# Kernel optimization log

Hardware: AMD Instinct MI355X
Metric: run time of the kernel (lower is better)

The kernel has to match this reference:

```python
import jax, jax.numpy as jnp
import numpy as np

N_HEADS = 32
KV_HEADS = 8
HEAD_DIM = 64
THETA = 10000.0


def _rope_tables(L, head_dim, dtype):
    freqs = 1.0 / (THETA ** (jnp.arange(0, head_dim, 2, dtype=jnp.float32) / head_dim))
    phases = jnp.outer(jnp.arange(L, dtype=jnp.float32), freqs)  # [L, head_dim//2]
    phases = jnp.concatenate([phases, phases], axis=-1)          # [L, head_dim]
    return jnp.cos(phases).astype(dtype), jnp.sin(phases).astype(dtype)


def _rotate_half(x):
    x1, x2 = jnp.split(x, 2, axis=-1)
    return jnp.concatenate([-x2, x1], axis=-1)


def setup_inputs() -> dict:
    key = jax.random.key(0)
    ks = jax.random.split(key, 5)
    B, L, D = 2, 2048, 2048
    kv_dim = KV_HEADS * HEAD_DIM
    s = 0.02
    return {
        "x": jax.random.normal(ks[0], (B, L, D), jnp.float32),
        "wq": jax.random.normal(ks[1], (D, D), jnp.float32) * s,
        "wk": jax.random.normal(ks[2], (kv_dim, D), jnp.float32) * s,
        "wv": jax.random.normal(ks[3], (kv_dim, D), jnp.float32) * s,
        "wo": jax.random.normal(ks[4], (D, D), jnp.float32) * s,
    }


def reference(x, wq, wk, wv, wo):
    B, L, D = x.shape
    rep = N_HEADS // KV_HEADS
    cos, sin = _rope_tables(L, HEAD_DIM, x.dtype)  # [L, hd]

    # projections (torch Linear: y = x @ W.T)
    q = jnp.einsum('bld,ed->ble', x, wq).reshape(B, L, N_HEADS, HEAD_DIM).transpose(0, 2, 1, 3)   # [B,H,L,hd]
    k = jnp.einsum('bld,ed->ble', x, wk).reshape(B, L, KV_HEADS, HEAD_DIM).transpose(0, 2, 1, 3)  # [B,Hk,L,hd]
    v = jnp.einsum('bld,ed->ble', x, wv).reshape(B, L, KV_HEADS, HEAD_DIM).transpose(0, 2, 1, 3)

    # RoPE (broadcast over batch/heads)
    q = cos * q + _rotate_half(q) * sin
    k = cos * k + _rotate_half(k) * sin

    # GQA attention without materializing repeated K/V: group query heads per kv head
    qg = q.reshape(B, KV_HEADS, rep, L, HEAD_DIM)
    scale = 1.0 / jnp.sqrt(jnp.asarray(HEAD_DIM, x.dtype))
    scores = jnp.einsum('bkrqd,bkld->bkrql', qg, k) * scale  # [B,Hk,rep,L,L]
    causal = jnp.tril(jnp.ones((L, L), bool))
    scores = jnp.where(causal, scores, jnp.asarray(-jnp.inf, scores.dtype))
    attn = jax.nn.softmax(scores, axis=-1)
    out = jnp.einsum('bkrql,bkld->bkrqd', attn, v)           # [B,Hk,rep,L,hd]
    out = out.reshape(B, N_HEADS, L, HEAD_DIM).transpose(0, 2, 1, 3).reshape(B, L, D)
    return jnp.einsum('ble,de->bld', out, wo)
```

## Files before the change

kernel.cpp:

```cpp
#include <hip/hip_runtime.h>

typedef __attribute__((ext_vector_type(8))) __bf16 bf16x8;
typedef __attribute__((ext_vector_type(8))) ushort u16x8;
typedef __attribute__((ext_vector_type(4))) float f32x4;
typedef __attribute__((ext_vector_type(16))) float f32x16;

#define MFMA16(a, b, c) __builtin_amdgcn_mfma_f32_16x16x32_bf16(a, b, c, 0, 0, 0)
#define MFMA32(a, b, c) __builtin_amdgcn_mfma_f32_32x32x16_bf16(a, b, c, 0, 0, 0)

__device__ __forceinline__ ushort f2bf(float f) {
    union { float f; unsigned u; } v; v.f = f;
    unsigned r = v.u + 0x7FFFu + ((v.u >> 16) & 1u);
    return (ushort)(r >> 16);
}
__device__ __forceinline__ float bf2f(ushort b) {
    union { unsigned u; float f; } v; v.u = ((unsigned)b) << 16; return v.f;
}
__device__ __forceinline__ int cvtpk(float lo, float hi) {
    int r; asm("v_cvt_pk_bf16_f32 %0, %1, %2" : "=v"(r) : "v"(lo), "v"(hi)); return r;
}
__device__ __forceinline__ float fexp2(float x) {
    float r; asm("v_exp_f32 %0, %1" : "=v"(r) : "v"(x)); return r;
}
__device__ __forceinline__ void gload_lds16(const void* g, void* l) {
    __builtin_amdgcn_global_load_lds((const __attribute__((address_space(1))) void*)g,
                                     (__attribute__((address_space(3))) void*)l, 16, 0, 0);
}

__device__ __forceinline__ int swz8(int row, int g) {
    return row * 64 + (((g) ^ (row & 7)) << 3);
}
__device__ __forceinline__ int swz16(int row, int g) {
    return row * 128 + (((g) ^ (row & 15)) << 3);
}

__device__ __forceinline__ void stage64(const ushort* __restrict__ g, int rs,
                                        char* lds, int tid) {
    const int r = tid >> 3;
    const int c8 = ((tid & 7) ^ (r & 7)) << 3;
    const int wid = tid >> 6;
    gload_lds16(g + (size_t)r * rs + c8, lds + wid * 1024);
    gload_lds16(g + (size_t)(r + 32) * rs + c8, lds + 4096 + wid * 1024);
}

__device__ __forceinline__ void stageV128(const ushort* __restrict__ g, char* lds, int tid) {
    const int w = tid >> 6, l = tid & 63;
    const int g16 = l & 15;
#pragma unroll
    for (int j = 0; j < 4; ++j) {
        const int r = w * 16 + j * 4 + (l >> 4);
        gload_lds16(g + (size_t)r * 2048 + ((g16 ^ (r & 15)) << 3), lds + w * 4096 + j * 1024);
    }
}

__global__ void cvt_all(const float* __restrict__ x,  const float* __restrict__ wq,
                        const float* __restrict__ wk, const float* __restrict__ wv,
                        const float* __restrict__ wo, ushort* __restrict__ xb,
                        ushort* __restrict__ wcat, ushort* __restrict__ wob,
                        float* __restrict__ cosT, float* __restrict__ sinT) {
    int i = blockIdx.x * 256 + threadIdx.x;
    if (i >= 4718592) {
        int id = i - 4718592;
        if (id < 65536) {
            int fi = id >> 11, l = id & 2047;
            float freq = __expf(-(float)fi * (9.210340371976184f / 32.0f));
            float ph = (float)l * freq;
            cosT[id] = cosf(ph);
            sinT[id] = sinf(ph);
        }
        return;
    }
    const float* src; ushort* dst; int off;
    if (i < 2097152)      { src = x;  dst = xb;             off = i; }
    else if (i < 3145728) { src = wq; dst = wcat;           off = i - 2097152; }
    else if (i < 3407872) { src = wk; dst = wcat + 4194304; off = i - 3145728; }
    else if (i < 3670016) { src = wv; dst = wcat + 5242880; off = i - 3407872; }
    else                  { src = wo; dst = wob;            off = i - 3670016; }
    float4 v = ((const float4*)src)[off];
    ushort4 o;
    o.x = f2bf(v.x); o.y = f2bf(v.y); o.z = f2bf(v.z); o.w = f2bf(v.w);
    ((ushort4*)dst)[off] = o;
}

__global__ __launch_bounds__(512, 2) void gemmQKV(const ushort* __restrict__ A,
                                                  const ushort* __restrict__ B,
                                                  ushort* __restrict__ qkv,
                                                  ushort* __restrict__ vt,
                                                  const float* __restrict__ cosT,
                                                  const float* __restrict__ sinT,
                                                  int M, int N, int K, int gx) {
    constexpr int MF = 8, NF = 4;
    constexpr int ABUF = 256 * 32, BBUF = 256 * 32;
    extern __shared__ __align__(16) ushort sm[];
    ushort* sA = sm;
    ushort* sB = sm + 3 * ABUF;
    const int tid = threadIdx.x, lane = tid & 63, wid = tid >> 6;
    const int wr = wid >> 2, wc = wid & 3;
    const int lr = lane & 15, lg = lane >> 4;
    const int nwg = gridDim.x, bid = blockIdx.x;
    const int swz = (bid & 7) * (nwg >> 3) + (bid >> 3);
    const int m0 = (swz / gx) * 256, n0 = (swz % gx) * 256;
    const int NT = K >> 5;
    const int csrc = ((tid & 3) ^ ((tid >> 3) & 3)) << 3;
    const int co = ((lg ^ ((lr >> 1) & 3)) << 3);
    const ushort* gAt = A + (size_t)(m0 + (tid >> 2)) * K + csrc;
    const ushort* gBt = B + (size_t)(n0 + (tid >> 2)) * K + csrc;

    auto stgA = [&](int t, int buf) {
        const ushort* g = gAt + t * 32;
        char* ld = (char*)(sA + buf * ABUF) + wid * 1024;
        gload_lds16(g, ld);
        gload_lds16(g + (size_t)128 * K, ld + 8192);
    };
    auto stgB = [&](int t, int buf) {
        const ushort* g = gBt + t * 32;
        char* ld = (char*)(sB + buf * BBUF) + wid * 1024;
        gload_lds16(g, ld);
        gload_lds16(g + (size_t)128 * K, ld + 8192);
    };

    f32x4 acc[MF][NF] = {};
    stgA(0, 0); stgB(0, 0); stgA(1, 1); stgB(1, 1);
    asm volatile("s_waitcnt vmcnt(4)" ::: "memory");
    __builtin_amdgcn_s_barrier();

    int cur = 0, stg = 2;
    for (int t = 0; t < NT; ++t) {
        const ushort* Ac = sA + cur * ABUF + (wr * 128) * 32 + co;
        const ushort* Bc = sB + cur * BBUF + (wc * 64) * 32 + co;
        bf16x8 bfr[NF], af[MF / 2];
#pragma unroll
        for (int nf = 0; nf < NF; ++nf) bfr[nf] = *(const bf16x8*)&Bc[(nf * 16 + lr) * 32];
#pragma unroll
        for (int mf = 0; mf < MF / 2; ++mf) af[mf] = *(const bf16x8*)&Ac[(mf * 16 + lr) * 32];
        if (t + 2 < NT) stgA(t + 2, stg);
        __builtin_amdgcn_s_barrier();
        __builtin_amdgcn_s_setprio(1);
#pragma unroll
        for (int mf = 0; mf < MF / 2; ++mf)
#pragma unroll
            for (int nf = 0; nf < NF; ++nf)
                acc[mf][nf] = MFMA16(af[mf], bfr[nf], acc[mf][nf]);
        __builtin_amdgcn_s_setprio(0);
        __builtin_amdgcn_s_barrier();
        bf16x8 af2[MF / 2];
#pragma unroll
        for (int mf = 0; mf < MF / 2; ++mf)
            af2[mf] = *(const bf16x8*)&Ac[((mf + MF / 2) * 16 + lr) * 32];
        if (t + 2 < NT) {
            stgB(t + 2, stg);
            asm volatile("s_waitcnt vmcnt(4)" ::: "memory");
        } else {
            asm volatile("s_waitcnt vmcnt(0)" ::: "memory");
        }
        __builtin_amdgcn_s_barrier();
        __builtin_amdgcn_s_setprio(1);
#pragma unroll
        for (int mf = 0; mf < MF / 2; ++mf)
#pragma unroll
            for (int nf = 0; nf < NF; ++nf)
                acc[mf + MF / 2][nf] = MFMA16(af2[mf], bfr[nf], acc[mf + MF / 2][nf]);
        __builtin_amdgcn_s_setprio(0);
        __builtin_amdgcn_s_barrier();
        cur = (cur == 2) ? 0 : cur + 1;
        stg = (stg == 2) ? 0 : stg + 1;
    }

    const int r0 = m0 + wr * 128 + lg * 4;
    const int c0 = n0 + wc * 64 + lr;
    const int wavecol = n0 + wc * 64;
    if (wavecol >= 2560) {
        const int kh = (wavecol - 2560) >> 6;
        const int b = m0 >> 11;
        const int l0 = r0 & 2047;
#pragma unroll
        for (int ni = 0; ni < NF; ++ni) {
            const int d = lr + ni * 16;
            ushort* vrow = vt + (size_t)((b * 8 + kh) * 64 + d) * 2048 + l0;
#pragma unroll
            for (int mi = 0; mi < MF; ++mi) {
                ushort4 o;
                o.x = f2bf(acc[mi][ni][0]); o.y = f2bf(acc[mi][ni][1]);
                o.z = f2bf(acc[mi][ni][2]); o.w = f2bf(acc[mi][ni][3]);
                *(ushort4*)(vrow + mi * 16) = o;
            }
        }
    } else {
        const float scale = (wavecol < 2048) ? 0.18033688f : 1.0f;
        const int l0 = r0 & 2047;
#pragma unroll
        for (int ni = 0; ni < NF / 2; ++ni) {
            const int i = ni * 16 + lr;
            const float* cp = cosT + i * 2048 + l0;
            const float* sp = sinT + i * 2048 + l0;
#pragma unroll
            for (int mi = 0; mi < MF; ++mi) {
                float4 cv = *(const float4*)(cp + mi * 16);
                float4 sv = *(const float4*)(sp + mi * 16);
#pragma unroll
                for (int r = 0; r < 4; ++r) {
                    float lo = acc[mi][ni][r], hi = acc[mi][ni + 2][r];
                    float c = ((const float*)&cv)[r], s = ((const float*)&sv)[r];
                    size_t row = (size_t)(r0 + mi * 16 + r) * 3072;
                    qkv[row + c0 + ni * 16]      = f2bf((c * lo - s * hi) * scale);
                    qkv[row + c0 + ni * 16 + 32] = f2bf((c * hi + s * lo) * scale);
                }
            }
        }
    }
}

__global__ __launch_bounds__(512, 2) void gemm64(const ushort* __restrict__ A,
                                                 const ushort* __restrict__ B,
                                                 float* __restrict__ C,
                                                 int M, int N, int K, int gx) {
    extern __shared__ __align__(16) ushort sm[];
    ushort* sA = sm;
    ushort* sB = sm + 32768;
    const int tid = threadIdx.x, lane = tid & 63, wid = tid >> 6;
    const int wr = wid >> 1, wc = wid & 1;
    const int lr = lane & 15, lg = lane >> 4;
    const int nwg = gridDim.x, bid = blockIdx.x;
    const int swz = (bid & 7) * (nwg >> 3) + (bid >> 3);
    const int m0 = (swz / gx) * 256, n0 = (swz % gx) * 128;
    const int NT = K >> 6;
    const int sr = tid >> 3;
    const int sc8 = ((tid & 7) ^ (sr & 7)) << 3;
    const ushort* gAt = A + (size_t)(m0 + sr) * K + sc8;
    const ushort* gBt = B + (size_t)(n0 + sr) * K + sc8;

    auto stgA = [&](int t, int buf) {
        const ushort* g = gAt + t * 64;
        char* ld = (char*)(sA + buf * 16384) + wid * 1024;
#pragma unroll
        for (int s = 0; s < 4; ++s)
            gload_lds16(g + (size_t)(s * 64) * K, ld + s * 8192);
    };
    auto stgB = [&](int t, int buf) {
        const ushort* g = gBt + t * 64;
        char* ld = (char*)(sB + buf * 8192) + wid * 1024;
        gload_lds16(g, ld);
        gload_lds16(g + (size_t)64 * K, ld + 8192);
    };

    f32x4 acc[4][4] = {};
    stgA(0, 0); stgB(0, 0);
    stgA(1, 1); stgB(1, 1);
    asm volatile("s_waitcnt vmcnt(6)" ::: "memory");
    __builtin_amdgcn_s_barrier();

    for (int t = 0; t < NT; ++t) {
        const int c = t & 1;
        const ushort* Ac = sA + c * 16384 + (wr * 64) * 64;
        const ushort* Bc = sB + c * 8192 + (wc * 64) * 64;
        bf16x8 af[4][2], bfr[4][2];
#pragma unroll
        for (int mf = 0; mf < 4; ++mf)
#pragma unroll
            for (int kk = 0; kk < 2; ++kk)
                af[mf][kk] = *(const bf16x8*)&Ac[swz8(mf * 16 + lr, kk * 4 + lg)];
#pragma unroll
        for (int nf = 0; nf < 4; ++nf)
#pragma unroll
            for (int kk = 0; kk < 2; ++kk)
                bfr[nf][kk] = *(const bf16x8*)&Bc[swz8(nf * 16 + lr, kk * 4 + lg)];
        __builtin_amdgcn_s_setprio(1);
#pragma unroll
        for (int mf = 0; mf < 4; ++mf)
#pragma unroll
            for (int nf = 0; nf < 4; ++nf)
#pragma unroll
                for (int kk = 0; kk < 2; ++kk)
                    acc[mf][nf] = MFMA16(af[mf][kk], bfr[nf][kk], acc[mf][nf]);
        __builtin_amdgcn_s_setprio(0);
        __builtin_amdgcn_s_barrier();
        if (t + 2 < NT) {
            stgA(t + 2, c); stgB(t + 2, c);
            asm volatile("s_waitcnt vmcnt(6)" ::: "memory");
        } else {
            asm volatile("s_waitcnt vmcnt(0)" ::: "memory");
        }
        __builtin_amdgcn_s_barrier();
    }

    const int r0 = m0 + wr * 64 + lg * 4;
    const int c0 = n0 + wc * 64 + lr;
#pragma unroll
    for (int mi = 0; mi < 4; ++mi)
#pragma unroll
        for (int ni = 0; ni < 4; ++ni)
#pragma unroll
            for (int r = 0; r < 4; ++r)
                C[(size_t)(r0 + mi * 16 + r) * N + c0 + ni * 16] = acc[mi][ni][r];
}

__global__ __launch_bounds__(256, 2) void attn_k(const ushort* __restrict__ qkv,
                                                 const ushort* __restrict__ vt,
                                                 ushort* __restrict__ attn) {
    extern __shared__ __align__(16) ushort smem[];
    const int tid = threadIdx.x, lane = tid & 63, wid = tid >> 6;
    const int hl = lane >> 5, lq = lane & 31;
    const int p = blockIdx.x;
    const int head = blockIdx.y, b = blockIdx.z;
    const int kh = head >> 2;

    const ushort* Kg = qkv + (size_t)(b * 2048) * 3072 + 2048 + kh * 64;
    const ushort* Vg = vt + (size_t)((b * 8 + kh) * 64) * 2048;

    for (int ph = 0; ph < 2; ++ph) {
        const int qt = ph ? p : 15 - p;
        const int qb = qt << 7;
        const int qw0 = qb + wid * 32;
        const int q_lane = qw0 + lq;
        const int nt = qt + 1;

        bf16x8 qf[4];
        {
            const ushort* qp = qkv + (size_t)(b * 2048 + qw0 + lq) * 3072 + head * 64 + hl * 8;
#pragma unroll
            for (int j = 0; j < 4; ++j) qf[j] = *(const bf16x8*)(qp + j * 16);
        }
        f32x16 o0 = {}, o1 = {};
        float lsum = 0.f;

        stage64(Kg, 3072, (char*)smem, tid);
        stage64(Kg + (size_t)64 * 3072, 3072, (char*)smem + 8192, tid);
        stageV128(Vg, (char*)(smem + 16384), tid);

        for (int it = 0; it < nt; ++it) {
            const int c = it & 1;
            const int kv0 = it << 7;
            const ushort* Kc = smem + c * 8192;
            const ushort* Vc = smem + 16384 + c * 8192;
            if (it + 1 < nt) {
                const int kv1 = kv0 + 128;
                char* kd = (char*)smem + (c ^ 1) * 16384;
                char* vd = (char*)(smem + 16384) + (c ^ 1) * 16384;
                stage64(Kg + (size_t)kv1 * 3072, 3072, kd, tid);
                stage64(Kg + (size_t)(kv1 + 64) * 3072, 3072, kd + 8192, tid);
                stageV128(Vg + kv1, vd, tid);
                asm volatile("s_waitcnt vmcnt(8)" ::: "memory");
            } else {
                asm volatile("s_waitcnt vmcnt(0)" ::: "memory");
            }
            __builtin_amdgcn_s_barrier();

            f32x16 s0 = {}, s1 = {}, s2 = {}, s3 = {};
            __builtin_amdgcn_s_setprio(1);
#pragma unroll
            for (int j = 0; j < 4; ++j) {
                bf16x8 k0 = *(const bf16x8*)&Kc[swz8(lq, j * 2 + hl)];
                bf16x8 k1 = *(const bf16x8*)&Kc[swz8(32 + lq, j * 2 + hl)];
                bf16x8 k2 = *(const bf16x8*)&Kc[swz8(64 + lq, j * 2 + hl)];
                bf16x8 k3 = *(const bf16x8*)&Kc[swz8(96 + lq, j * 2 + hl)];
                s0 = MFMA32(k0, qf[j], s0);
                s1 = MFMA32(k1, qf[j], s1);
                s2 = MFMA32(k2, qf[j], s2);
                s3 = MFMA32(k3, qf[j], s3);
            }
            __builtin_amdgcn_s_setprio(0);

            if (it == qt) {
#pragma unroll
                for (int i = 0; i < 16; ++i) {
                    int r = (i & 3) + ((i >> 2) << 3) + (hl << 2) + kv0;
                    if (r > q_lane)      s0[i] = -1e30f;
                    if (r + 32 > q_lane) s1[i] = -1e30f;
                    if (r + 64 > q_lane) s2[i] = -1e30f;
                    if (r + 96 > q_lane) s3[i] = -1e30f;
                }
            }
#pragma unroll
            for (int i = 0; i < 16; ++i) s0[i] = fexp2(s0[i]);
#pragma unroll
            for (int i = 0; i < 16; ++i) s1[i] = fexp2(s1[i]);
#pragma unroll
            for (int i = 0; i < 16; ++i) s2[i] = fexp2(s2[i]);
#pragma unroll
            for (int i = 0; i < 16; ++i) s3[i] = fexp2(s3[i]);
            f32x16 ts = (s0 + s1) + (s2 + s3);
            float u0 = ts[0] + ts[1], u1 = ts[2] + ts[3], u2 = ts[4] + ts[5], u3 = ts[6] + ts[7];
            float u4 = ts[8] + ts[9], u5 = ts[10] + ts[11], u6 = ts[12] + ts[13], u7 = ts[14] + ts[15];
            float rs = ((u0 + u1) + (u2 + u3)) + ((u4 + u5) + (u6 + u7));
            {
                auto sw = __builtin_amdgcn_permlane32_swap(__float_as_int(rs), __float_as_int(rs), 0, 0);
                rs = __int_as_float(sw[0]) + __int_as_float(sw[1]);
            }
            lsum += rs;

            bf16x8 pf[8];
#define PFB(cc, q0, q1, q2, q3, q4, q5, q6, q7)                                   \
            {                                                                      \
                int pk01 = cvtpk(q0, q1), pk23 = cvtpk(q2, q3);                    \
                int pk45 = cvtpk(q4, q5), pk67 = cvtpk(q6, q7);                    \
                auto sA = __builtin_amdgcn_permlane32_swap(pk01, pk45, 0, 0);      \
                auto sB = __builtin_amdgcn_permlane32_swap(pk23, pk67, 0, 0);      \
                union { int w[4]; bf16x8 v; } u;                                   \
                u.w[0] = sA[0]; u.w[1] = sB[0]; u.w[2] = sA[1]; u.w[3] = sB[1];    \
                pf[cc] = u.v;                                                      \
            }
            PFB(0, s0[0], s0[1], s0[2], s0[3], s0[4], s0[5], s0[6], s0[7])
            PFB(1, s0[8], s0[9], s0[10], s0[11], s0[12], s0[13], s0[14], s0[15])
            PFB(2, s1[0], s1[1], s1[2], s1[3], s1[4], s1[5], s1[6], s1[7])
            PFB(3, s1[8], s1[9], s1[10], s1[11], s1[12], s1[13], s1[14], s1[15])
            PFB(4, s2[0], s2[1], s2[2], s2[3], s2[4], s2[5], s2[6], s2[7])
            PFB(5, s2[8], s2[9], s2[10], s2[11], s2[12], s2[13], s2[14], s2[15])
            PFB(6, s3[0], s3[1], s3[2], s3[3], s3[4], s3[5], s3[6], s3[7])
            PFB(7, s3[8], s3[9], s3[10], s3[11], s3[12], s3[13], s3[14], s3[15])
#undef PFB
            __builtin_amdgcn_s_setprio(1);
#pragma unroll
            for (int cc = 0; cc < 8; ++cc) {
                bf16x8 v0 = *(const bf16x8*)&Vc[swz16(lq, cc * 2 + hl)];
                bf16x8 v1 = *(const bf16x8*)&Vc[swz16(32 + lq, cc * 2 + hl)];
                o0 = MFMA32(v0, pf[cc], o0);
                o1 = MFMA32(v1, pf[cc], o1);
            }
            __builtin_amdgcn_s_setprio(0);
            __builtin_amdgcn_s_barrier();
        }

        __syncthreads();
        ushort* sc = (ushort*)((char*)smem + wid * 4096);
        float inv = 1.0f / lsum;
#pragma unroll
        for (int i = 0; i < 16; i += 2) {
            int d0 = (i & 3) + ((i >> 2) << 3) + (hl << 2);
            int g0 = d0 >> 3, g1 = (d0 + 32) >> 3;
            *(int*)&sc[lq * 64 + ((g0 ^ (lq & 7)) << 3) + (d0 & 7)] = cvtpk(o0[i] * inv, o0[i + 1] * inv);
            *(int*)&sc[lq * 64 + ((g1 ^ (lq & 7)) << 3) + (d0 & 7)] = cvtpk(o1[i] * inv, o1[i + 1] * inv);
        }
        __syncthreads();
        {
            const int q = lane >> 1, db = (lane & 1) << 5;
            const size_t orow = (size_t)(b * 2048 + qb + wid * 32 + q);
#pragma unroll
            for (int j = 0; j < 4; ++j) {
                int g = (db >> 3) + j;
                u16x8 v = *(const u16x8*)&sc[q * 64 + ((g ^ (q & 7)) << 3)];
                *(u16x8*)(attn + orow * 2048 + head * 64 + g * 8) = v;
            }
        }
        __syncthreads();
    }
}

extern "C" void kernel_launch(void* const* d_in, const int* in_sizes, int n_in,
                              void* d_out, int out_size, void* d_ws, size_t ws_size,
                              hipStream_t stream) {
    const float* x  = (const float*)d_in[0];
    const float* wq = (const float*)d_in[1];
    const float* wk = (const float*)d_in[2];
    const float* wv = (const float*)d_in[3];
    const float* wo = (const float*)d_in[4];
    float* out = (float*)d_out;
    char* ws = (char*)d_ws;

    ushort* xb   = (ushort*)(ws);
    ushort* wcat = (ushort*)(ws + 16777216);
    ushort* wob  = (ushort*)(ws + 29360128);
    ushort* qkv  = (ushort*)(ws + 37748736);
    ushort* vt   = (ushort*)(ws + 62914560);
    ushort* attn = (ushort*)(ws + 67108864);
    float*  cosT = (float*)(ws + 83886080);
    float*  sinT = (float*)(ws + 84148224);

    (void)hipFuncSetAttribute((const void*)gemmQKV,
                              hipFuncAttributeMaxDynamicSharedMemorySize, 98304);
    (void)hipFuncSetAttribute((const void*)gemm64,
                              hipFuncAttributeMaxDynamicSharedMemorySize, 98304);
    (void)hipFuncSetAttribute((const void*)attn_k,
                              hipFuncAttributeMaxDynamicSharedMemorySize, 65536);

    cvt_all<<<18688, 256, 0, stream>>>(x, wq, wk, wv, wo, xb, wcat, wob, cosT, sinT);
    gemmQKV<<<192, 512, 98304, stream>>>(xb, wcat, qkv, vt, cosT, sinT, 4096, 3072, 2048, 12);
    attn_k<<<dim3(8, 32, 2), 256, 65536, stream>>>(qkv, vt, attn);
    gemm64<<<256, 512, 98304, stream>>>(attn, wob, out, 4096, 2048, 2048, 16);
}
```

Before: 172.4 us.

## Restructure QKV GEMM to K-step 64 with double-buffered LDS pipeline

The fused QKV projection GEMM now consumes 64-wide K tiles instead of 32, using two LDS buffers instead of three and an XOR swizzle over 8 chunks. Each iteration issues twice as many MFMAs between barriers and prefetches both A and B two stages ahead after the compute, halving the number of loop iterations and barriers. LDS use grows to 128 KB per block, so only one block fits per CU despite the launch bound of 2, which trades occupancy for fewer synchronisations.

```diff
diff --git a/kernel.cpp b/kernel.cpp
--- a/kernel.cpp
+++ b/kernel.cpp
@@ -82,88 +82,97 @@
     ((ushort4*)dst)[off] = o;
 }
 
-__global__ __launch_bounds__(512, 2) void gemmQKV(const ushort* __restrict__ A,
-                                                  const ushort* __restrict__ B,
-                                                  ushort* __restrict__ qkv,
-                                                  ushort* __restrict__ vt,
-                                                  const float* __restrict__ cosT,
-                                                  const float* __restrict__ sinT,
-                                                  int M, int N, int K, int gx) {
-    constexpr int MF = 8, NF = 4;
-    constexpr int ABUF = 256 * 32, BBUF = 256 * 32;
+__global__ __launch_bounds__(512, 2) void gemmQKV64(const ushort* __restrict__ A,
+                                                    const ushort* __restrict__ B,
+                                                    ushort* __restrict__ qkv,
+                                                    ushort* __restrict__ vt,
+                                                    const float* __restrict__ cosT,
+                                                    const float* __restrict__ sinT,
+                                                    int K, int gx) {
     extern __shared__ __align__(16) ushort sm[];
     ushort* sA = sm;
-    ushort* sB = sm + 3 * ABUF;
+    ushort* sB = sm + 32768;
     const int tid = threadIdx.x, lane = tid & 63, wid = tid >> 6;
     const int wr = wid >> 2, wc = wid & 3;
     const int lr = lane & 15, lg = lane >> 4;
     const int nwg = gridDim.x, bid = blockIdx.x;
     const int swz = (bid & 7) * (nwg >> 3) + (bid >> 3);
     const int m0 = (swz / gx) * 256, n0 = (swz % gx) * 256;
-    const int NT = K >> 5;
-    const int csrc = ((tid & 3) ^ ((tid >> 3) & 3)) << 3;
-    const int co = ((lg ^ ((lr >> 1) & 3)) << 3);
-    const ushort* gAt = A + (size_t)(m0 + (tid >> 2)) * K + csrc;
-    const ushort* gBt = B + (size_t)(n0 + (tid >> 2)) * K + csrc;
+    const int NT = K >> 6;
+    const int sr = tid >> 3;
+    const int sc8 = ((tid & 7) ^ (sr & 7)) << 3;
+    const ushort* gAt = A + (size_t)(m0 + sr) * K + sc8;
+    const ushort* gBt = B + (size_t)(n0 + sr) * K + sc8;
 
     auto stgA = [&](int t, int buf) {
-        const ushort* g = gAt + t * 32;
-        char* ld = (char*)(sA + buf * ABUF) + wid * 1024;
-        gload_lds16(g, ld);
-        gload_lds16(g + (size_t)128 * K, ld + 8192);
+        const ushort* g = gAt + t * 64;
+        char* ld = (char*)(sA + buf * 16384) + wid * 1024;
+#pragma unroll
+        for (int s = 0; s < 4; ++s)
+            gload_lds16(g + (size_t)(s * 64) * K, ld + s * 8192);
     };
     auto stgB = [&](int t, int buf) {
-        const ushort* g = gBt + t * 32;
-        char* ld = (char*)(sB + buf * BBUF) + wid * 1024;
-        gload_lds16(g, ld);
-        gload_lds16(g + (size_t)128 * K, ld + 8192);
+        const ushort* g = gBt + t * 64;
+        char* ld = (char*)(sB + buf * 16384) + wid * 1024;
+#pragma unroll
+        for (int s = 0; s < 4; ++s)
+            gload_lds16(g + (size_t)(s * 64) * K, ld + s * 8192);
     };
 
-    f32x4 acc[MF][NF] = {};
-    stgA(0, 0); stgB(0, 0); stgA(1, 1); stgB(1, 1);
-    asm volatile("s_waitcnt vmcnt(4)" ::: "memory");
+    f32x4 acc[8][4] = {};
+    stgA(0, 0); stgB(0, 0);
+    stgA(1, 1); stgB(1, 1);
+    asm volatile("s_waitcnt vmcnt(8)" ::: "memory");
     __builtin_amdgcn_s_barrier();
 
-    int cur = 0, stg = 2;
     for (int t = 0; t < NT; ++t) {
-        const ushort* Ac = sA + cur * ABUF + (wr * 128) * 32 + co;
-        const ushort* Bc = sB + cur * BBUF + (wc * 64) * 32 + co;
-        bf16x8 bfr[NF], af[MF / 2];
-#pragma unroll
-        for (int nf = 0; nf < NF; ++nf) bfr[nf] = *(const bf16x8*)&Bc[(nf * 16 + lr) * 32];
-#pragma unroll
-        for (int mf = 0; mf < MF / 2; ++mf) af[mf] = *(const bf16x8*)&Ac[(mf * 16 + lr) * 32];
-        if (t + 2 < NT) stgA(t + 2, stg);
-        __builtin_amdgcn_s_barrier();
+        const int c = t & 1;
+        const ushort* Ac = sA + c * 16384 + (wr * 128) * 64;
+        const ushort* Bc = sB + c * 16384 + (wc * 64) * 64;
+        bf16x8 bfr[4][2];
+#pragma unroll
+        for (int nf = 0; nf < 4; ++nf)
+#pragma unroll
+            for (int kk = 0; kk < 2; ++kk)
+                bfr[nf][kk] = *(const bf16x8*)&Bc[swz8(nf * 16 + lr, kk * 4 + lg)];
+        bf16x8 af[4][2];
+#pragma unroll
+        for (int mf = 0; mf < 4; ++mf)
+#pragma unroll
+            for (int kk = 0; kk < 2; ++kk)
+                af[mf][kk] = *(const bf16x8*)&Ac[swz8(mf * 16 + lr, kk * 4 + lg)];
         __builtin_amdgcn_s_setprio(1);
 #pragma unroll
-        for (int mf = 0; mf < MF / 2; ++mf)
-#pragma unroll
-            for (int nf = 0; nf < NF; ++nf)
-                acc[mf][nf] = MFMA16(af[mf], bfr[nf], acc[mf][nf]);
+        for (int mf = 0; mf < 4; ++mf)
+#pragma unroll
+            for (int nf = 0; nf < 4; ++nf)
+#pragma unroll
+                for (int kk = 0; kk < 2; ++kk)
+                    acc[mf][nf] = MFMA16(af[mf][kk], bfr[nf][kk], acc[mf][nf]);
+        __builtin_amdgcn_s_setprio(0);
+        bf16x8 af2[4][2];
+#pragma unroll
+        for (int mf = 0; mf < 4; ++mf)
+#pragma unroll
+            for (int kk = 0; kk < 2; ++kk)
+                af2[mf][kk] = *(const bf16x8*)&Ac[swz8((mf + 4) * 16 + lr, kk * 4 + lg)];
+        __builtin_amdgcn_s_setprio(1);
+#pragma unroll
+        for (int mf = 0; mf < 4; ++mf)
+#pragma unroll
+            for (int nf = 0; nf < 4; ++nf)
+#pragma unroll
+                for (int kk = 0; kk < 2; ++kk)
+                    acc[mf + 4][nf] = MFMA16(af2[mf][kk], bfr[nf][kk], acc[mf + 4][nf]);
         __builtin_amdgcn_s_setprio(0);
         __builtin_amdgcn_s_barrier();
-        bf16x8 af2[MF / 2];
-#pragma unroll
-        for (int mf = 0; mf < MF / 2; ++mf)
-            af2[mf] = *(const bf16x8*)&Ac[((mf + MF / 2) * 16 + lr) * 32];
         if (t + 2 < NT) {
-            stgB(t + 2, stg);
-            asm volatile("s_waitcnt vmcnt(4)" ::: "memory");
+            stgA(t + 2, c); stgB(t + 2, c);
+            asm volatile("s_waitcnt vmcnt(8)" ::: "memory");
         } else {
             asm volatile("s_waitcnt vmcnt(0)" ::: "memory");
         }
         __builtin_amdgcn_s_barrier();
-        __builtin_amdgcn_s_setprio(1);
-#pragma unroll
-        for (int mf = 0; mf < MF / 2; ++mf)
-#pragma unroll
-            for (int nf = 0; nf < NF; ++nf)
-                acc[mf + MF / 2][nf] = MFMA16(af2[mf], bfr[nf], acc[mf + MF / 2][nf]);
-        __builtin_amdgcn_s_setprio(0);
-        __builtin_amdgcn_s_barrier();
-        cur = (cur == 2) ? 0 : cur + 1;
-        stg = (stg == 2) ? 0 : stg + 1;
     }
 
     const int r0 = m0 + wr * 128 + lg * 4;
@@ -174,11 +183,11 @@
         const int b = m0 >> 11;
         const int l0 = r0 & 2047;
 #pragma unroll
-        for (int ni = 0; ni < NF; ++ni) {
+        for (int ni = 0; ni < 4; ++ni) {
             const int d = lr + ni * 16;
             ushort* vrow = vt + (size_t)((b * 8 + kh) * 64 + d) * 2048 + l0;
 #pragma unroll
-            for (int mi = 0; mi < MF; ++mi) {
+            for (int mi = 0; mi < 8; ++mi) {
                 ushort4 o;
                 o.x = f2bf(acc[mi][ni][0]); o.y = f2bf(acc[mi][ni][1]);
                 o.z = f2bf(acc[mi][ni][2]); o.w = f2bf(acc[mi][ni][3]);
@@ -189,12 +198,12 @@
         const float scale = (wavecol < 2048) ? 0.18033688f : 1.0f;
         const int l0 = r0 & 2047;
 #pragma unroll
-        for (int ni = 0; ni < NF / 2; ++ni) {
+        for (int ni = 0; ni < 2; ++ni) {
             const int i = ni * 16 + lr;
             const float* cp = cosT + i * 2048 + l0;
             const float* sp = sinT + i * 2048 + l0;
 #pragma unroll
-            for (int mi = 0; mi < MF; ++mi) {
+            for (int mi = 0; mi < 8; ++mi) {
                 float4 cv = *(const float4*)(cp + mi * 16);
                 float4 sv = *(const float4*)(sp + mi * 16);
 #pragma unroll
@@ -465,15 +474,15 @@
     float*  cosT = (float*)(ws + 83886080);
     float*  sinT = (float*)(ws + 84148224);
 
-    (void)hipFuncSetAttribute((const void*)gemmQKV,
-                              hipFuncAttributeMaxDynamicSharedMemorySize, 98304);
+    (void)hipFuncSetAttribute((const void*)gemmQKV64,
+                              hipFuncAttributeMaxDynamicSharedMemorySize, 131072);
     (void)hipFuncSetAttribute((const void*)gemm64,
                               hipFuncAttributeMaxDynamicSharedMemorySize, 98304);
     (void)hipFuncSetAttribute((const void*)attn_k,
                               hipFuncAttributeMaxDynamicSharedMemorySize, 65536);
 
     cvt_all<<<18688, 256, 0, stream>>>(x, wq, wk, wv, wo, xb, wcat, wob, cosT, sinT);
-    gemmQKV<<<192, 512, 98304, stream>>>(xb, wcat, qkv, vt, cosT, sinT, 4096, 3072, 2048, 12);
+    gemmQKV64<<<192, 512, 131072, stream>>>(xb, wcat, qkv, vt, cosT, sinT, 2048, 12);
     attn_k<<<dim3(8, 32, 2), 256, 65536, stream>>>(qkv, vt, attn);
     gemm64<<<256, 512, 98304, stream>>>(attn, wob, out, 4096, 2048, 2048, 16);
 }
```

Measured after the change: 175.5 us. Within noise of the previous version (+1.8%).
